# Performance work log

Measured on AMD Instinct MI355X. Metric: run time of the kernel, lower is better.

## Reference

```python
import math
import jax, jax.numpy as jnp
import numpy as np


def _alibi_slopes(n_heads: int) -> np.ndarray:
    def pow2_slopes(n):
        start = 2 ** (-2 ** (-(math.log2(n) - 3)))
        return [start * (start ** i) for i in range(n)]
    if n_heads & (n_heads - 1) == 0:
        slopes = pow2_slopes(n_heads)
    else:
        closest = 2 ** math.floor(math.log2(n_heads))
        slopes = pow2_slopes(closest)
        extra_base = 2 ** (-2 ** (-(math.log2(2 * closest) - 3)))
        slopes.extend(extra_base * (extra_base ** i) for i in range(n_heads - closest))
        slopes = slopes[:n_heads]
    return np.asarray(slopes, dtype=np.float32)


def setup_inputs() -> dict:
    B, T, C, H = 2, 2048, 768, 12
    key = jax.random.key(0)
    ks = jax.random.split(key, 6)
    return {
        "x_norm_for_qk": jax.random.normal(ks[0], (B, T, C), jnp.float32),
        "xt_current_for_v": jax.random.normal(ks[1], (B, T, C), jnp.float32),
        "W_attn": jax.random.normal(ks[2], (2 * C, C), jnp.float32) * 0.02,  # nn.Linear weight [out,in]
        "b_attn": jnp.zeros((2 * C,), jnp.float32),
        "v_tmp": jax.random.normal(ks[3], (H, H), jnp.float32) * 0.02,
        "proj_tmp": jax.random.normal(ks[4], (H, H), jnp.float32) * 0.02,
    }


def reference(x_norm_for_qk, xt_current_for_v, W_attn, b_attn, v_tmp, proj_tmp):
    B, T, C = x_norm_for_qk.shape
    H = v_tmp.shape[0]
    hd = C // H

    # Q,K projection: Linear(C -> 2C), then split.
    qk = x_norm_for_qk @ W_attn.T + b_attn  # [B,T,2C]
    q, k = jnp.split(qk, 2, axis=-1)
    q = q.reshape(B, T, H, hd).transpose(0, 2, 1, 3)  # [B,H,T,hd]
    k = k.reshape(B, T, H, hd).transpose(0, 2, 1, 3)

    # Kronecker-lifted V: block (i,j) of the CxC matrix is v_tmp[i,j]*I(hd),
    # so applying it mixes only across heads per head-dim channel.
    xt = xt_current_for_v.reshape(B, T, H, hd)
    v = jnp.einsum("ij,btjd->btid", v_tmp, xt).transpose(0, 2, 1, 3)  # [B,H,T,hd]

    scale = 1.0 / math.sqrt(hd)
    scores = jnp.einsum("bhqd,bhkd->bhqk", q, k) * scale  # [B,H,T,T]

    # ALiBi bias with causal mask (-inf above diagonal).
    slopes = jnp.asarray(_alibi_slopes(H))  # [H]
    pos = jnp.arange(T, dtype=jnp.float32)
    rel = pos[None, :] - pos[:, None]  # [T,T], memory - context
    causal = pos[None, :] <= pos[:, None]
    bias = jnp.where(causal[None], slopes[:, None, None] * rel[None], -jnp.inf)  # [H,T,T]
    scores = scores + bias[None]

    att = jax.nn.softmax(scores, axis=-1)  # dropout p=0 -> identity
    y = jnp.einsum("bhqk,bhkd->bhqd", att, v)  # [B,H,T,hd]
    y = y.transpose(0, 2, 1, 3)  # [B,T,H,hd]

    # Kronecker-lifted output projection.
    y = jnp.einsum("ij,btjd->btid", proj_tmp, y)
    return y.reshape(B, T, C)
```

## Files before the change

### kernel.cpp

```cpp
#include <hip/hip_runtime.h>
#include <hip/hip_bf16.h>
#include <math.h>

#define TSEQ 2048
#define CDIM 768
#define NH   12
#define HD   64

typedef __attribute__((ext_vector_type(8))) short bf16x8;
typedef __attribute__((ext_vector_type(4))) float f32x4;

union Bf8 { bf16x8 v; __hip_bfloat16 e[8]; };

__constant__ float c_slopes2[12] = {
    0.72134752f, 0.36067376f, 0.18033688f, 0.09016844f,
    0.04508422f, 0.02254211f, 0.011271055f, 0.0056355275f,
    1.02015692f, 0.72134752f, 0.51007846f, 0.36067376f
};
#define M2 4.3280851f
#define QSCALE 0.18033688f
#define EXP2F(x) __builtin_amdgcn_exp2f(x)

__device__ __forceinline__ unsigned pack2(float lo, float hi) {
    union { __hip_bfloat162 b; unsigned u; } cv;
    cv.b = __float22bfloat162_rn(make_float2(lo, hi));
    return cv.u;
}
__device__ __forceinline__ unsigned short bf16bits(float x) {
    union { __hip_bfloat16 b; unsigned short s; } cv;
    cv.b = __float2bfloat16(x);
    return cv.s;
}

#define MFMA16(a, b, c) __builtin_amdgcn_mfma_f32_16x16x32_bf16(a, b, c, 0, 0, 0)

__global__ __launch_bounds__(256) void gemm_qk(
    const float* __restrict__ X,
    const float* __restrict__ W,
    const float* __restrict__ bias,
    __hip_bfloat16* __restrict__ Qb,
    __hip_bfloat16* __restrict__ Kt)
{
    __shared__ alignas(16) __hip_bfloat16 As[128][40];
    __shared__ alignas(16) __hip_bfloat16 Bs[64][40];

    const int tid  = threadIdx.x;
    const int lane = tid & 63;
    const int w    = tid >> 6;
    const int lg   = lane >> 4;
    const int lc   = lane & 15;
    const int m0   = blockIdx.y * 128;
    const int n0   = blockIdx.x * 64;
    const int m0w  = (w >> 1) * 64;
    const int n0w  = (w & 1) * 32;

    const int r0 = tid >> 2;
    const int c0 = (tid & 3) * 8;

    f32x4 acc[4][2] = {};

    for (int k0 = 0; k0 < CDIM; k0 += 32) {
        __syncthreads();
        {
            const float* xp0 = X + (size_t)(m0 + r0) * CDIM + k0 + c0;
            const float* xp1 = X + (size_t)(m0 + r0 + 64) * CDIM + k0 + c0;
            const float* wp  = W + (size_t)(n0 + r0) * CDIM + k0 + c0;
            float4 a00 = *(const float4*)(xp0);
            float4 a01 = *(const float4*)(xp0 + 4);
            float4 a10 = *(const float4*)(xp1);
            float4 a11 = *(const float4*)(xp1 + 4);
            float4 b0  = *(const float4*)(wp);
            float4 b1  = *(const float4*)(wp + 4);
            Bf8 v0, v1, bv;
            v0.e[0]=__float2bfloat16(a00.x); v0.e[1]=__float2bfloat16(a00.y);
            v0.e[2]=__float2bfloat16(a00.z); v0.e[3]=__float2bfloat16(a00.w);
            v0.e[4]=__float2bfloat16(a01.x); v0.e[5]=__float2bfloat16(a01.y);
            v0.e[6]=__float2bfloat16(a01.z); v0.e[7]=__float2bfloat16(a01.w);
            v1.e[0]=__float2bfloat16(a10.x); v1.e[1]=__float2bfloat16(a10.y);
            v1.e[2]=__float2bfloat16(a10.z); v1.e[3]=__float2bfloat16(a10.w);
            v1.e[4]=__float2bfloat16(a11.x); v1.e[5]=__float2bfloat16(a11.y);
            v1.e[6]=__float2bfloat16(a11.z); v1.e[7]=__float2bfloat16(a11.w);
            bv.e[0]=__float2bfloat16(b0.x);  bv.e[1]=__float2bfloat16(b0.y);
            bv.e[2]=__float2bfloat16(b0.z);  bv.e[3]=__float2bfloat16(b0.w);
            bv.e[4]=__float2bfloat16(b1.x);  bv.e[5]=__float2bfloat16(b1.y);
            bv.e[6]=__float2bfloat16(b1.z);  bv.e[7]=__float2bfloat16(b1.w);
            *(bf16x8*)&As[r0][c0]      = v0.v;
            *(bf16x8*)&As[r0 + 64][c0] = v1.v;
            *(bf16x8*)&Bs[r0][c0]      = bv.v;
        }
        __syncthreads();

        bf16x8 af[4], bfr[2];
        #pragma unroll
        for (int mt = 0; mt < 4; ++mt)
            af[mt] = *(const bf16x8*)&As[m0w + mt*16 + lc][lg*8];
        #pragma unroll
        for (int nt = 0; nt < 2; ++nt)
            bfr[nt] = *(const bf16x8*)&Bs[n0w + nt*16 + lc][lg*8];
        #pragma unroll
        for (int mt = 0; mt < 4; ++mt)
            #pragma unroll
            for (int nt = 0; nt < 2; ++nt)
                acc[mt][nt] = MFMA16(af[mt], bfr[nt], acc[mt][nt]);
    }

    #pragma unroll
    for (int mt = 0; mt < 4; ++mt) {
        #pragma unroll
        for (int nt = 0; nt < 2; ++nt) {
            int n  = n0 + n0w + nt*16 + lc;
            float bv = bias[n];
            #pragma unroll
            for (int r = 0; r < 4; ++r) {
                int m = m0 + m0w + mt*16 + lg*4 + r;
                float v = acc[mt][nt][r] + bv;
                int b = m >> 11, t = m & (TSEQ-1);
                if (n < CDIM) {
                    int h = n >> 6, dd = n & 63;
                    Qb[(((size_t)(b*NH + h))*TSEQ + t)*HD + dd] = __float2bfloat16(v * QSCALE);
                } else {
                    int n2 = n - CDIM;
                    int h = n2 >> 6, dd = n2 & 63;
                    int bh_ = b*NH + h;
                    int kb = t >> 5, tt = t & 31;
                    int j  = ((tt >> 4) << 1) + (dd >> 5);
                    int ln = (((dd >> 3) & 3) << 4) + (tt & 15);
                    Kt[((size_t)(bh_*64 + kb))*2048 + j*512 + ln*8 + (dd & 7)] =
                        __float2bfloat16(v);
                }
            }
        }
    }
}

__global__ __launch_bounds__(256) void vmix(
    const float* __restrict__ XT, const float* __restrict__ vtmp,
    __hip_bfloat16* __restrict__ Vb)
{
    __shared__ float vm[144];
    if (threadIdx.x < 144) vm[threadIdx.x] = vtmp[threadIdx.x];
    __syncthreads();
    int idx = blockIdx.x * 256 + threadIdx.x;
    int dd = idx & 63;
    int bt = idx >> 6;
    int t = bt & (TSEQ-1), b = bt >> 11;
    float xv[12];
    #pragma unroll
    for (int j = 0; j < 12; ++j) xv[j] = XT[(size_t)bt*CDIM + j*64 + dd];
    #pragma unroll
    for (int i = 0; i < 12; ++i) {
        float s = 0.f;
        #pragma unroll
        for (int j = 0; j < 12; ++j) s += vm[i*12+j] * xv[j];
        Vb[(((size_t)(b*NH + i))*TSEQ + t)*HD + dd] = __float2bfloat16(s);
    }
}

__global__ __launch_bounds__(256) void vtrans(
    const __hip_bfloat16* __restrict__ Vb, __hip_bfloat16* __restrict__ Vt)
{
    __shared__ __hip_bfloat16 Ls[64][65];
    const int bh = blockIdx.y;
    const int t0 = blockIdx.x * 64;
    const int tid = threadIdx.x;
    const int r8 = tid >> 3;
    const int c8 = (tid & 7) * 8;

    #pragma unroll
    for (int it = 0; it < 2; ++it) {
        int t = it*32 + r8;
        Bf8 v; v.v = *(const bf16x8*)(Vb + ((size_t)bh*TSEQ + t0 + t)*HD + c8);
        #pragma unroll
        for (int j = 0; j < 8; ++j) Ls[t][c8 + j] = v.e[j];
    }
    __syncthreads();
    #pragma unroll
    for (int it = 0; it < 2; ++it) {
        int d = it*32 + r8;
        Bf8 v;
        #pragma unroll
        for (int j = 0; j < 8; ++j) v.e[j] = Ls[c8 + j][d];
        int kb = (t0 + c8) >> 5;
        int ko = (t0 + c8) & 31;
        *(bf16x8*)(Vt + (size_t)bh*(HD*TSEQ) + kb*2048 + d*32 + ko) = v.v;
    }
}

__global__ __launch_bounds__(256, 3) void attn8(
    const __hip_bfloat16* __restrict__ Qb,
    const __hip_bfloat16* __restrict__ Kt,
    const __hip_bfloat16* __restrict__ Vt,
    __hip_bfloat16* __restrict__ Y)
{
    __shared__ float Osh[4][2][64][20];
    __shared__ float Lsh[4][2][16];

    const int tid  = threadIdx.x;
    const int lane = tid & 63;
    const int w    = tid >> 6;
    const int lg   = lane >> 4;
    const int lc   = lane & 15;

    const int id  = blockIdx.x;
    const int id2 = (id & 7) * 96 + (id >> 3);
    const int bx  = id2 & 31;
    const int bh  = id2 >> 5;

    const float slope = c_slopes2[bh % NH];
    const __hip_bfloat16* Qp = Qb + (size_t)bh * TSEQ * HD;
    const __hip_bfloat16* Kp = Kt + (size_t)bh * 64 * 2048;
    const __hip_bfloat16* Vp = Vt + (size_t)bh * (HD * TSEQ);

    const float slgl  = slope * (float)(lg * 4);
    const float slp16 = slope * 16.0f;
    const int   s01   = lc + ((lg & 1) << 5);
    const int   s23   = s01 + 16;
    const bool  hiK   = (lg >= 2);

    bf16x8 kA0, kA1, kA2, kA3, kB0, kB1, kB2, kB3;

#define LOADK(S, TI) do {                                                       \
    const __hip_bfloat16* kp_ = Kp + (size_t)(TI)*2048 + lane*8;                \
    k##S##0 = *(const bf16x8*)(kp_);                                            \
    k##S##1 = *(const bf16x8*)(kp_ + 512);                                      \
    k##S##2 = *(const bf16x8*)(kp_ + 1024);                                     \
    k##S##3 = *(const bf16x8*)(kp_ + 1536);                                     \
} while (0);

#define SHUF(P_, x0, x1, x2, x3)                                                \
    {                                                                           \
        int t00 = __shfl((int)x0, s01), t02 = __shfl((int)x2, s01);             \
        int t10 = __shfl((int)x1, s01), t12 = __shfl((int)x3, s01);             \
        int t20 = __shfl((int)x0, s23), t22 = __shfl((int)x2, s23);             \
        int t30 = __shfl((int)x1, s23), t32 = __shfl((int)x3, s23);             \
        P_.u[0] = hiK ? (unsigned)t02 : (unsigned)t00;                          \
        P_.u[1] = hiK ? (unsigned)t12 : (unsigned)t10;                          \
        P_.u[2] = hiK ? (unsigned)t22 : (unsigned)t20;                          \
        P_.u[3] = hiK ? (unsigned)t32 : (unsigned)t30;                          \
    }

#define CONS(TI, S) do {                                                        \
    const int K0C = (TI) * 32;                                                  \
    const __hip_bfloat16* vb_ = Vp + (size_t)(TI)*2048 + lc*32 + lg*8;          \
    bf16x8 v0_ = *(const bf16x8*)(vb_);                                         \
    bf16x8 v1_ = *(const bf16x8*)(vb_ + 512);                                   \
    bf16x8 v2_ = *(const bf16x8*)(vb_ + 1024);                                  \
    bf16x8 v3_ = *(const bf16x8*)(vb_ + 1536);                                  \
    f32x4 s0a = {}, s0b = {}, s1a = {}, s1b = {};                               \
    s0a = MFMA16(k##S##0, qfa0, s0a); s0a = MFMA16(k##S##1, qfa1, s0a);         \
    s0b = MFMA16(k##S##0, qfb0, s0b); s0b = MFMA16(k##S##1, qfb1, s0b);         \
    s1a = MFMA16(k##S##2, qfa0, s1a); s1a = MFMA16(k##S##3, qfa1, s1a);         \
    s1b = MFMA16(k##S##2, qfb0, s1b); s1b = MFMA16(k##S##3, qfb1, s1b);         \
    float base0_ = fmaf((float)K0C, slope, slgl);                               \
    float pa0[4], pa1[4], pb0[4], pb1[4];                                       \
    _Pragma("unroll")                                                           \
    for (int r = 0; r < 4; ++r) {                                               \
        float bk_  = base0_ + slope * (float)r;                                 \
        float bk1_ = bk_ + slp16;                                               \
        int kk0_ = K0C + lg*4 + r, kk1_ = kk0_ + 16;                            \
        float e0a = EXP2F(s0a[r] + (bk_  - eqa));                               \
        float e1a = EXP2F(s1a[r] + (bk1_ - eqa));                               \
        float e0b = EXP2F(s0b[r] + (bk_  - eqb));                               \
        float e1b = EXP2F(s1b[r] + (bk1_ - eqb));                               \
        pa0[r] = (kk0_ <= qia) ? e0a : 0.f;                                     \
        pa1[r] = (kk1_ <= qia) ? e1a : 0.f;                                     \
        pb0[r] = (kk0_ <= qib) ? e0b : 0.f;                                     \
        pb1[r] = (kk1_ <= qib) ? e1b : 0.f;                                     \
        lsa += pa0[r] + pa1[r];                                                 \
        lsb += pb0[r] + pb1[r];                                                 \
    }                                                                           \
    unsigned a0_ = pack2(pa0[0], pa0[1]), a1_ = pack2(pa0[2], pa0[3]);          \
    unsigned a2_ = pack2(pa1[0], pa1[1]), a3_ = pack2(pa1[2], pa1[3]);          \
    unsigned b0_ = pack2(pb0[0], pb0[1]), b1_ = pack2(pb0[2], pb0[3]);          \
    unsigned b2_ = pack2(pb1[0], pb1[1]), b3_ = pack2(pb1[2], pb1[3]);          \
    union { unsigned u[4]; bf16x8 v; } PA_, PB_;                                \
    SHUF(PA_, a0_, a1_, a2_, a3_)                                               \
    SHUF(PB_, b0_, b1_, b2_, b3_)                                               \
    Oa[0] = MFMA16(v0_, PA_.v, Oa[0]); Ob[0] = MFMA16(v0_, PB_.v, Ob[0]);       \
    Oa[1] = MFMA16(v1_, PA_.v, Oa[1]); Ob[1] = MFMA16(v1_, PB_.v, Ob[1]);       \
    Oa[2] = MFMA16(v2_, PA_.v, Oa[2]); Ob[2] = MFMA16(v2_, PB_.v, Ob[2]);       \
    Oa[3] = MFMA16(v3_, PA_.v, Oa[3]); Ob[3] = MFMA16(v3_, PB_.v, Ob[3]);       \
} while (0);

    auto runMember = [&](int qb, bool first) {
        const int q0m = qb * 32;
        const int qia = q0m + lc;
        const int qib = q0m + 16 + lc;
        const float eqa = slope * (float)qia + M2;
        const float eqb = slope * (float)qib + M2;

        bf16x8 qfa0 = *(const bf16x8*)(Qp + (size_t)qia * HD + lg*8);
        bf16x8 qfa1 = *(const bf16x8*)(Qp + (size_t)qia * HD + 32 + lg*8);
        bf16x8 qfb0 = *(const bf16x8*)(Qp + (size_t)qib * HD + lg*8);
        bf16x8 qfb1 = *(const bf16x8*)(Qp + (size_t)qib * HD + 32 + lg*8);

        f32x4 Oa[4] = {}; f32x4 Ob[4] = {};
        float lsa = 0.f, lsb = 0.f;

        const int myN = (qb >= w) ? ((qb - w) >> 2) + 1 : 0;

        if (myN > 0) {
            LOADK(A, w)
            int j = 0;
            while (true) {
                if (j + 1 < myN) LOADK(B, w + 4*(j+1))
                CONS(w + 4*j, A)
                ++j; if (j >= myN) break;
                if (j + 1 < myN) LOADK(A, w + 4*(j+1))
                CONS(w + 4*j, B)
                ++j; if (j >= myN) break;
            }
        }

        lsa += __shfl_xor(lsa, 16); lsa += __shfl_xor(lsa, 32);
        lsb += __shfl_xor(lsb, 16); lsb += __shfl_xor(lsb, 32);

        if (!first) __syncthreads();
        #pragma unroll
        for (int dt = 0; dt < 4; ++dt) {
            *(f32x4*)&Osh[w][0][lane][dt*4] = Oa[dt];
            *(f32x4*)&Osh[w][1][lane][dt*4] = Ob[dt];
        }
        if (lane < 16) {
            Lsh[w][0][lane] = lsa;
            Lsh[w][1][lane] = lsb;
        }
        __syncthreads();

        #pragma unroll
        for (int h = 0; h < 2; ++h) {
            f32x4 o = (h == 0) ? Oa[w] : Ob[w];
            #pragma unroll
            for (int w2 = 0; w2 < 4; ++w2)
                if (w2 != w) o += *(const f32x4*)&Osh[w2][h][lane][w*4];
            float lt = Lsh[0][h][lc] + Lsh[1][h][lc] + Lsh[2][h][lc] + Lsh[3][h][lc];
            float inv = 1.0f / lt;
            int q = q0m + h*16 + lc;
            ushort4 u;
            u.x = bf16bits(o[0] * inv);
            u.y = bf16bits(o[1] * inv);
            u.z = bf16bits(o[2] * inv);
            u.w = bf16bits(o[3] * inv);
            *(ushort4*)(Y + ((size_t)bh*TSEQ + q)*HD + w*16 + lg*4) = u;
        }
    };

    runMember(bx, true);
    runMember(63 - bx, false);

#undef LOADK
#undef SHUF
#undef CONS
}

__global__ __launch_bounds__(256) void projmix(
    const __hip_bfloat16* __restrict__ Y, const float* __restrict__ ptmp,
    float* __restrict__ Out)
{
    __shared__ float pm[144];
    if (threadIdx.x < 144) pm[threadIdx.x] = ptmp[threadIdx.x];
    __syncthreads();
    int idx = blockIdx.x * 256 + threadIdx.x;
    int dd = idx & 63;
    int bt = idx >> 6;
    int t = bt & (TSEQ-1), b = bt >> 11;
    float yv[12];
    #pragma unroll
    for (int j = 0; j < 12; ++j)
        yv[j] = __bfloat162float(Y[(((size_t)(b*NH + j))*TSEQ + t)*HD + dd]);
    #pragma unroll
    for (int i = 0; i < 12; ++i) {
        float s = 0.f;
        #pragma unroll
        for (int j = 0; j < 12; ++j) s += pm[i*12+j] * yv[j];
        Out[(size_t)bt*CDIM + i*64 + dd] = s;
    }
}

extern "C" void kernel_launch(void* const* d_in, const int* in_sizes, int n_in,
                              void* d_out, int out_size, void* d_ws, size_t ws_size,
                              hipStream_t stream) {
    (void)in_sizes; (void)n_in; (void)out_size; (void)ws_size;
    const float* X    = (const float*)d_in[0];
    const float* XT   = (const float*)d_in[1];
    const float* W    = (const float*)d_in[2];
    const float* bias = (const float*)d_in[3];
    const float* vtmp = (const float*)d_in[4];
    const float* ptmp = (const float*)d_in[5];
    float* Out = (float*)d_out;

    char* ws = (char*)d_ws;
    const size_t BHTD = (size_t)2 * NH * TSEQ * HD;
    __hip_bfloat16* Qb = (__hip_bfloat16*)ws;
    __hip_bfloat16* Kt = (__hip_bfloat16*)(ws + BHTD*2);
    __hip_bfloat16* Vb = (__hip_bfloat16*)(ws + BHTD*4);
    __hip_bfloat16* Vt = (__hip_bfloat16*)(ws + BHTD*6);
    __hip_bfloat16* Yb = (__hip_bfloat16*)(ws + BHTD*8);

    gemm_qk<<<dim3(24, 32), 256, 0, stream>>>(X, W, bias, Qb, Kt);
    vmix<<<1024, 256, 0, stream>>>(XT, vtmp, Vb);
    vtrans<<<dim3(32, 24), 256, 0, stream>>>(Vb, Vt);
    attn8<<<768, 256, 0, stream>>>(Qb, Kt, Vt, Yb);
    projmix<<<1024, 256, 0, stream>>>(Yb, ptmp, Out);
}
```

Measured before the change: 81.91 us.

## Fuse QK GEMM, V mixing and transpose into one prep kernel; split attention blocks

After: 197.1 us. +140.6%, slower.

```diff
diff --git a/kernel.cpp b/kernel.cpp
--- a/kernel.cpp
+++ b/kernel.cpp
@@ -34,177 +34,173 @@
 
 #define MFMA16(a, b, c) __builtin_amdgcn_mfma_f32_16x16x32_bf16(a, b, c, 0, 0, 0)
 
-__global__ __launch_bounds__(256) void gemm_qk(
+__global__ __launch_bounds__(256) void prep(
     const float* __restrict__ X,
     const float* __restrict__ W,
     const float* __restrict__ bias,
+    const float* __restrict__ XT,
+    const float* __restrict__ vtmp,
     __hip_bfloat16* __restrict__ Qb,
-    __hip_bfloat16* __restrict__ Kt)
+    __hip_bfloat16* __restrict__ Kt,
+    __hip_bfloat16* __restrict__ Vt)
 {
     __shared__ alignas(16) __hip_bfloat16 As[128][40];
     __shared__ alignas(16) __hip_bfloat16 Bs[64][40];
+    __shared__ float vm[144];
+
+    const int bid = blockIdx.x;
+    const int tid = threadIdx.x;
+
+    if (bid < 768) {
+        const int lane = tid & 63;
+        const int w    = tid >> 6;
+        const int lg   = lane >> 4;
+        const int lc   = lane & 15;
+        const int m0   = (bid / 24) * 128;
+        const int n0   = (bid % 24) * 64;
+        const int m0w  = (w >> 1) * 64;
+        const int n0w  = (w & 1) * 32;
+
+        const int r0 = tid >> 2;
+        const int c0 = (tid & 3) * 8;
+
+        f32x4 acc[4][2] = {};
+
+        for (int k0 = 0; k0 < CDIM; k0 += 32) {
+            __syncthreads();
+            {
+                const float* xp0 = X + (size_t)(m0 + r0) * CDIM + k0 + c0;
+                const float* xp1 = X + (size_t)(m0 + r0 + 64) * CDIM + k0 + c0;
+                const float* wp  = W + (size_t)(n0 + r0) * CDIM + k0 + c0;
+                float4 a00 = *(const float4*)(xp0);
+                float4 a01 = *(const float4*)(xp0 + 4);
+                float4 a10 = *(const float4*)(xp1);
+                float4 a11 = *(const float4*)(xp1 + 4);
+                float4 b0  = *(const float4*)(wp);
+                float4 b1  = *(const float4*)(wp + 4);
+                Bf8 v0, v1, bv;
+                v0.e[0]=__float2bfloat16(a00.x); v0.e[1]=__float2bfloat16(a00.y);
+                v0.e[2]=__float2bfloat16(a00.z); v0.e[3]=__float2bfloat16(a00.w);
+                v0.e[4]=__float2bfloat16(a01.x); v0.e[5]=__float2bfloat16(a01.y);
+                v0.e[6]=__float2bfloat16(a01.z); v0.e[7]=__float2bfloat16(a01.w);
+                v1.e[0]=__float2bfloat16(a10.x); v1.e[1]=__float2bfloat16(a10.y);
+                v1.e[2]=__float2bfloat16(a10.z); v1.e[3]=__float2bfloat16(a10.w);
+                v1.e[4]=__float2bfloat16(a11.x); v1.e[5]=__float2bfloat16(a11.y);
+                v1.e[6]=__float2bfloat16(a11.z); v1.e[7]=__float2bfloat16(a11.w);
+                bv.e[0]=__float2bfloat16(b0.x);  bv.e[1]=__float2bfloat16(b0.y);
+                bv.e[2]=__float2bfloat16(b0.z);  bv.e[3]=__float2bfloat16(b0.w);
+                bv.e[4]=__float2bfloat16(b1.x);  bv.e[5]=__float2bfloat16(b1.y);
+                bv.e[6]=__float2bfloat16(b1.z);  bv.e[7]=__float2bfloat16(b1.w);
+                *(bf16x8*)&As[r0][c0]      = v0.v;
+                *(bf16x8*)&As[r0 + 64][c0] = v1.v;
+                *(bf16x8*)&Bs[r0][c0]      = bv.v;
+            }
+            __syncthreads();
+
+            bf16x8 af[4], bfr[2];
+            #pragma unroll
+            for (int mt = 0; mt < 4; ++mt)
+                af[mt] = *(const bf16x8*)&As[m0w + mt*16 + lc][lg*8];
+            #pragma unroll
+            for (int nt = 0; nt < 2; ++nt)
+                bfr[nt] = *(const bf16x8*)&Bs[n0w + nt*16 + lc][lg*8];
+            #pragma unroll
+            for (int mt = 0; mt < 4; ++mt)
+                #pragma unroll
+                for (int nt = 0; nt < 2; ++nt)
+                    acc[mt][nt] = MFMA16(af[mt], bfr[nt], acc[mt][nt]);
+        }
+
+        #pragma unroll
+        for (int mt = 0; mt < 4; ++mt) {
+            #pragma unroll
+            for (int nt = 0; nt < 2; ++nt) {
+                int n  = n0 + n0w + nt*16 + lc;
+                float bv = bias[n];
+                #pragma unroll
+                for (int r = 0; r < 4; ++r) {
+                    int m = m0 + m0w + mt*16 + lg*4 + r;
+                    float v = acc[mt][nt][r] + bv;
+                    int b = m >> 11, t = m & (TSEQ-1);
+                    if (n < CDIM) {
+                        int h = n >> 6, dd = n & 63;
+                        Qb[(((size_t)(b*NH + h))*TSEQ + t)*HD + dd] = __float2bfloat16(v * QSCALE);
+                    } else {
+                        int n2 = n - CDIM;
+                        int h = n2 >> 6, dd = n2 & 63;
+                        int bh_ = b*NH + h;
+                        int kb = t >> 5, tt = t & 31;
+                        int j  = ((tt >> 4) << 1) + (dd >> 5);
+                        int ln = (((dd >> 3) & 3) << 4) + (tt & 15);
+                        Kt[((size_t)(bh_*64 + kb))*2048 + j*512 + ln*8 + (dd & 7)] =
+                            __float2bfloat16(v);
+                    }
+                }
+            }
+        }
+    } else {
+        const int vb = bid - 768;
+        const int b  = vb >> 5;
+        const int t0 = (vb & 31) * 64;
+        const int tl = tid >> 2;
+        const int dq = tid & 3;
+
+        if (tid < 144) vm[tid] = vtmp[tid];
+        __syncthreads();
+
+        const int tg  = t0 + tl;
+        const size_t xbase = (size_t)(b*TSEQ + tg) * CDIM;
+        const int kb0 = tg >> 5;
+        const int ko  = tg & 31;
+
+        #pragma unroll
+        for (int c = 0; c < 4; ++c) {
+            const int dd0 = dq*16 + c*4;
+            float4 xv[12];
+            #pragma unroll
+            for (int j = 0; j < 12; ++j)
+                xv[j] = *(const float4*)(XT + xbase + j*64 + dd0);
+            #pragma unroll
+            for (int i = 0; i < 12; ++i) {
+                float ox = 0.f, oy = 0.f, oz = 0.f, ow = 0.f;
+                #pragma unroll
+                for (int j = 0; j < 12; ++j) {
+                    float s = vm[i*12 + j];
+                    ox = fmaf(s, xv[j].x, ox);
+                    oy = fmaf(s, xv[j].y, oy);
+                    oz = fmaf(s, xv[j].z, oz);
+                    ow = fmaf(s, xv[j].w, ow);
+                }
+                __hip_bfloat16* vt = Vt + (size_t)(b*NH + i)*(HD*TSEQ)
+                                       + (size_t)kb0*2048 + ko;
+                vt[(dd0+0)*32] = __float2bfloat16(ox);
+                vt[(dd0+1)*32] = __float2bfloat16(oy);
+                vt[(dd0+2)*32] = __float2bfloat16(oz);
+                vt[(dd0+3)*32] = __float2bfloat16(ow);
+            }
+        }
+    }
+}
+
+__global__ __launch_bounds__(256, 6) void attn11(
+    const __hip_bfloat16* __restrict__ Qb,
+    const __hip_bfloat16* __restrict__ Kt,
+    const __hip_bfloat16* __restrict__ Vt,
+    __hip_bfloat16* __restrict__ Y)
+{
+    __shared__ float Osh[4][64][20];
+    __shared__ float Lsh[4][16];
 
     const int tid  = threadIdx.x;
     const int lane = tid & 63;
     const int w    = tid >> 6;
     const int lg   = lane >> 4;
     const int lc   = lane & 15;
-    const int m0   = blockIdx.y * 128;
-    const int n0   = blockIdx.x * 64;
-    const int m0w  = (w >> 1) * 64;
-    const int n0w  = (w & 1) * 32;
-
-    const int r0 = tid >> 2;
-    const int c0 = (tid & 3) * 8;
-
-    f32x4 acc[4][2] = {};
-
-    for (int k0 = 0; k0 < CDIM; k0 += 32) {
-        __syncthreads();
-        {
-            const float* xp0 = X + (size_t)(m0 + r0) * CDIM + k0 + c0;
-            const float* xp1 = X + (size_t)(m0 + r0 + 64) * CDIM + k0 + c0;
-            const float* wp  = W + (size_t)(n0 + r0) * CDIM + k0 + c0;
-            float4 a00 = *(const float4*)(xp0);
-            float4 a01 = *(const float4*)(xp0 + 4);
-            float4 a10 = *(const float4*)(xp1);
-            float4 a11 = *(const float4*)(xp1 + 4);
-            float4 b0  = *(const float4*)(wp);
-            float4 b1  = *(const float4*)(wp + 4);
-            Bf8 v0, v1, bv;
-            v0.e[0]=__float2bfloat16(a00.x); v0.e[1]=__float2bfloat16(a00.y);
-            v0.e[2]=__float2bfloat16(a00.z); v0.e[3]=__float2bfloat16(a00.w);
-            v0.e[4]=__float2bfloat16(a01.x); v0.e[5]=__float2bfloat16(a01.y);
-            v0.e[6]=__float2bfloat16(a01.z); v0.e[7]=__float2bfloat16(a01.w);
-            v1.e[0]=__float2bfloat16(a10.x); v1.e[1]=__float2bfloat16(a10.y);
-            v1.e[2]=__float2bfloat16(a10.z); v1.e[3]=__float2bfloat16(a10.w);
-            v1.e[4]=__float2bfloat16(a11.x); v1.e[5]=__float2bfloat16(a11.y);
-            v1.e[6]=__float2bfloat16(a11.z); v1.e[7]=__float2bfloat16(a11.w);
-            bv.e[0]=__float2bfloat16(b0.x);  bv.e[1]=__float2bfloat16(b0.y);
-            bv.e[2]=__float2bfloat16(b0.z);  bv.e[3]=__float2bfloat16(b0.w);
-            bv.e[4]=__float2bfloat16(b1.x);  bv.e[5]=__float2bfloat16(b1.y);
-            bv.e[6]=__float2bfloat16(b1.z);  bv.e[7]=__float2bfloat16(b1.w);
-            *(bf16x8*)&As[r0][c0]      = v0.v;
-            *(bf16x8*)&As[r0 + 64][c0] = v1.v;
-            *(bf16x8*)&Bs[r0][c0]      = bv.v;
-        }
-        __syncthreads();
-
-        bf16x8 af[4], bfr[2];
-        #pragma unroll
-        for (int mt = 0; mt < 4; ++mt)
-            af[mt] = *(const bf16x8*)&As[m0w + mt*16 + lc][lg*8];
-        #pragma unroll
-        for (int nt = 0; nt < 2; ++nt)
-            bfr[nt] = *(const bf16x8*)&Bs[n0w + nt*16 + lc][lg*8];
-        #pragma unroll
-        for (int mt = 0; mt < 4; ++mt)
-            #pragma unroll
-            for (int nt = 0; nt < 2; ++nt)
-                acc[mt][nt] = MFMA16(af[mt], bfr[nt], acc[mt][nt]);
-    }
-
-    #pragma unroll
-    for (int mt = 0; mt < 4; ++mt) {
-        #pragma unroll
-        for (int nt = 0; nt < 2; ++nt) {
-            int n  = n0 + n0w + nt*16 + lc;
-            float bv = bias[n];
-            #pragma unroll
-            for (int r = 0; r < 4; ++r) {
-                int m = m0 + m0w + mt*16 + lg*4 + r;
-                float v = acc[mt][nt][r] + bv;
-                int b = m >> 11, t = m & (TSEQ-1);
-                if (n < CDIM) {
-                    int h = n >> 6, dd = n & 63;
-                    Qb[(((size_t)(b*NH + h))*TSEQ + t)*HD + dd] = __float2bfloat16(v * QSCALE);
-                } else {
-                    int n2 = n - CDIM;
-                    int h = n2 >> 6, dd = n2 & 63;
-                    int bh_ = b*NH + h;
-                    int kb = t >> 5, tt = t & 31;
-                    int j  = ((tt >> 4) << 1) + (dd >> 5);
-                    int ln = (((dd >> 3) & 3) << 4) + (tt & 15);
-                    Kt[((size_t)(bh_*64 + kb))*2048 + j*512 + ln*8 + (dd & 7)] =
-                        __float2bfloat16(v);
-                }
-            }
-        }
-    }
-}
-
-__global__ __launch_bounds__(256) void vmix(
-    const float* __restrict__ XT, const float* __restrict__ vtmp,
-    __hip_bfloat16* __restrict__ Vb)
-{
-    __shared__ float vm[144];
-    if (threadIdx.x < 144) vm[threadIdx.x] = vtmp[threadIdx.x];
-    __syncthreads();
-    int idx = blockIdx.x * 256 + threadIdx.x;
-    int dd = idx & 63;
-    int bt = idx >> 6;
-    int t = bt & (TSEQ-1), b = bt >> 11;
-    float xv[12];
-    #pragma unroll
-    for (int j = 0; j < 12; ++j) xv[j] = XT[(size_t)bt*CDIM + j*64 + dd];
-    #pragma unroll
-    for (int i = 0; i < 12; ++i) {
-        float s = 0.f;
-        #pragma unroll
-        for (int j = 0; j < 12; ++j) s += vm[i*12+j] * xv[j];
-        Vb[(((size_t)(b*NH + i))*TSEQ + t)*HD + dd] = __float2bfloat16(s);
-    }
-}
-
-__global__ __launch_bounds__(256) void vtrans(
-    const __hip_bfloat16* __restrict__ Vb, __hip_bfloat16* __restrict__ Vt)
-{
-    __shared__ __hip_bfloat16 Ls[64][65];
-    const int bh = blockIdx.y;
-    const int t0 = blockIdx.x * 64;
-    const int tid = threadIdx.x;
-    const int r8 = tid >> 3;
-    const int c8 = (tid & 7) * 8;
-
-    #pragma unroll
-    for (int it = 0; it < 2; ++it) {
-        int t = it*32 + r8;
-        Bf8 v; v.v = *(const bf16x8*)(Vb + ((size_t)bh*TSEQ + t0 + t)*HD + c8);
-        #pragma unroll
-        for (int j = 0; j < 8; ++j) Ls[t][c8 + j] = v.e[j];
-    }
-    __syncthreads();
-    #pragma unroll
-    for (int it = 0; it < 2; ++it) {
-        int d = it*32 + r8;
-        Bf8 v;
-        #pragma unroll
-        for (int j = 0; j < 8; ++j) v.e[j] = Ls[c8 + j][d];
-        int kb = (t0 + c8) >> 5;
-        int ko = (t0 + c8) & 31;
-        *(bf16x8*)(Vt + (size_t)bh*(HD*TSEQ) + kb*2048 + d*32 + ko) = v.v;
-    }
-}
-
-__global__ __launch_bounds__(256, 3) void attn8(
-    const __hip_bfloat16* __restrict__ Qb,
-    const __hip_bfloat16* __restrict__ Kt,
-    const __hip_bfloat16* __restrict__ Vt,
-    __hip_bfloat16* __restrict__ Y)
-{
-    __shared__ float Osh[4][2][64][20];
-    __shared__ float Lsh[4][2][16];
-
-    const int tid  = threadIdx.x;
-    const int lane = tid & 63;
-    const int w    = tid >> 6;
-    const int lg   = lane >> 4;
-    const int lc   = lane & 15;
 
     const int id  = blockIdx.x;
-    const int id2 = (id & 7) * 96 + (id >> 3);
-    const int bx  = id2 & 31;
-    const int bh  = id2 >> 5;
+    const int id2 = (id & 7) * 192 + (id >> 3);
+    const int qb  = 63 - (id2 & 63);
+    const int bh  = id2 >> 6;
 
     const float slope = c_slopes2[bh % NH];
     const __hip_bfloat16* Qp = Qb + (size_t)bh * TSEQ * HD;
@@ -217,140 +213,134 @@
     const int   s23   = s01 + 16;
     const bool  hiK   = (lg >= 2);
 
-    bf16x8 kA0, kA1, kA2, kA3, kB0, kB1, kB2, kB3;
-
-#define LOADK(S, TI) do {                                                       \
-    const __hip_bfloat16* kp_ = Kp + (size_t)(TI)*2048 + lane*8;                \
-    k##S##0 = *(const bf16x8*)(kp_);                                            \
-    k##S##1 = *(const bf16x8*)(kp_ + 512);                                      \
-    k##S##2 = *(const bf16x8*)(kp_ + 1024);                                     \
-    k##S##3 = *(const bf16x8*)(kp_ + 1536);                                     \
-} while (0);
-
-#define SHUF(P_, x0, x1, x2, x3)                                                \
-    {                                                                           \
-        int t00 = __shfl((int)x0, s01), t02 = __shfl((int)x2, s01);             \
-        int t10 = __shfl((int)x1, s01), t12 = __shfl((int)x3, s01);             \
-        int t20 = __shfl((int)x0, s23), t22 = __shfl((int)x2, s23);             \
-        int t30 = __shfl((int)x1, s23), t32 = __shfl((int)x3, s23);             \
-        P_.u[0] = hiK ? (unsigned)t02 : (unsigned)t00;                          \
-        P_.u[1] = hiK ? (unsigned)t12 : (unsigned)t10;                          \
-        P_.u[2] = hiK ? (unsigned)t22 : (unsigned)t20;                          \
-        P_.u[3] = hiK ? (unsigned)t32 : (unsigned)t30;                          \
-    }
-
-#define CONS(TI, S) do {                                                        \
-    const int K0C = (TI) * 32;                                                  \
-    const __hip_bfloat16* vb_ = Vp + (size_t)(TI)*2048 + lc*32 + lg*8;          \
-    bf16x8 v0_ = *(const bf16x8*)(vb_);                                         \
-    bf16x8 v1_ = *(const bf16x8*)(vb_ + 512);                                   \
-    bf16x8 v2_ = *(const bf16x8*)(vb_ + 1024);                                  \
-    bf16x8 v3_ = *(const bf16x8*)(vb_ + 1536);                                  \
-    f32x4 s0a = {}, s0b = {}, s1a = {}, s1b = {};                               \
-    s0a = MFMA16(k##S##0, qfa0, s0a); s0a = MFMA16(k##S##1, qfa1, s0a);         \
-    s0b = MFMA16(k##S##0, qfb0, s0b); s0b = MFMA16(k##S##1, qfb1, s0b);         \
-    s1a = MFMA16(k##S##2, qfa0, s1a); s1a = MFMA16(k##S##3, qfa1, s1a);         \
-    s1b = MFMA16(k##S##2, qfb0, s1b); s1b = MFMA16(k##S##3, qfb1, s1b);         \
-    float base0_ = fmaf((float)K0C, slope, slgl);                               \
-    float pa0[4], pa1[4], pb0[4], pb1[4];                                       \
-    _Pragma("unroll")                                                           \
-    for (int r = 0; r < 4; ++r) {                                               \
-        float bk_  = base0_ + slope * (float)r;                                 \
-        float bk1_ = bk_ + slp16;                                               \
-        int kk0_ = K0C + lg*4 + r, kk1_ = kk0_ + 16;                            \
-        float e0a = EXP2F(s0a[r] + (bk_  - eqa));                               \
-        float e1a = EXP2F(s1a[r] + (bk1_ - eqa));                               \
-        float e0b = EXP2F(s0b[r] + (bk_  - eqb));                               \
-        float e1b = EXP2F(s1b[r] + (bk1_ - eqb));                               \
-        pa0[r] = (kk0_ <= qia) ? e0a : 0.f;                                     \
-        pa1[r] = (kk1_ <= qia) ? e1a : 0.f;                                     \
-        pb0[r] = (kk0_ <= qib) ? e0b : 0.f;                                     \
-        pb1[r] = (kk1_ <= qib) ? e1b : 0.f;                                     \
-        lsa += pa0[r] + pa1[r];                                                 \
-        lsb += pb0[r] + pb1[r];                                                 \
-    }                                                                           \
-    unsigned a0_ = pack2(pa0[0], pa0[1]), a1_ = pack2(pa0[2], pa0[3]);          \
-    unsigned a2_ = pack2(pa1[0], pa1[1]), a3_ = pack2(pa1[2], pa1[3]);          \
-    unsigned b0_ = pack2(pb0[0], pb0[1]), b1_ = pack2(pb0[2], pb0[3]);          \
-    unsigned b2_ = pack2(pb1[0], pb1[1]), b3_ = pack2(pb1[2], pb1[3]);          \
-    union { unsigned u[4]; bf16x8 v; } PA_, PB_;                                \
-    SHUF(PA_, a0_, a1_, a2_, a3_)                                               \
-    SHUF(PB_, b0_, b1_, b2_, b3_)                                               \
-    Oa[0] = MFMA16(v0_, PA_.v, Oa[0]); Ob[0] = MFMA16(v0_, PB_.v, Ob[0]);       \
-    Oa[1] = MFMA16(v1_, PA_.v, Oa[1]); Ob[1] = MFMA16(v1_, PB_.v, Ob[1]);       \
-    Oa[2] = MFMA16(v2_, PA_.v, Oa[2]); Ob[2] = MFMA16(v2_, PB_.v, Ob[2]);       \
-    Oa[3] = MFMA16(v3_, PA_.v, Oa[3]); Ob[3] = MFMA16(v3_, PB_.v, Ob[3]);       \
-} while (0);
-
-    auto runMember = [&](int qb, bool first) {
-        const int q0m = qb * 32;
-        const int qia = q0m + lc;
-        const int qib = q0m + 16 + lc;
-        const float eqa = slope * (float)qia + M2;
-        const float eqb = slope * (float)qib + M2;
-
-        bf16x8 qfa0 = *(const bf16x8*)(Qp + (size_t)qia * HD + lg*8);
-        bf16x8 qfa1 = *(const bf16x8*)(Qp + (size_t)qia * HD + 32 + lg*8);
-        bf16x8 qfb0 = *(const bf16x8*)(Qp + (size_t)qib * HD + lg*8);
-        bf16x8 qfb1 = *(const bf16x8*)(Qp + (size_t)qib * HD + 32 + lg*8);
-
-        f32x4 Oa[4] = {}; f32x4 Ob[4] = {};
-        float lsa = 0.f, lsb = 0.f;
-
-        const int myN = (qb >= w) ? ((qb - w) >> 2) + 1 : 0;
-
-        if (myN > 0) {
-            LOADK(A, w)
-            int j = 0;
-            while (true) {
-                if (j + 1 < myN) LOADK(B, w + 4*(j+1))
-                CONS(w + 4*j, A)
-                ++j; if (j >= myN) break;
-                if (j + 1 < myN) LOADK(A, w + 4*(j+1))
-                CONS(w + 4*j, B)
-                ++j; if (j >= myN) break;
-            }
-        }
-
-        lsa += __shfl_xor(lsa, 16); lsa += __shfl_xor(lsa, 32);
-        lsb += __shfl_xor(lsb, 16); lsb += __shfl_xor(lsb, 32);
-
-        if (!first) __syncthreads();
-        #pragma unroll
-        for (int dt = 0; dt < 4; ++dt) {
-            *(f32x4*)&Osh[w][0][lane][dt*4] = Oa[dt];
-            *(f32x4*)&Osh[w][1][lane][dt*4] = Ob[dt];
-        }
-        if (lane < 16) {
-            Lsh[w][0][lane] = lsa;
-            Lsh[w][1][lane] = lsb;
-        }
-        __syncthreads();
-
-        #pragma unroll
-        for (int h = 0; h < 2; ++h) {
-            f32x4 o = (h == 0) ? Oa[w] : Ob[w];
-            #pragma unroll
-            for (int w2 = 0; w2 < 4; ++w2)
-                if (w2 != w) o += *(const f32x4*)&Osh[w2][h][lane][w*4];
-            float lt = Lsh[0][h][lc] + Lsh[1][h][lc] + Lsh[2][h][lc] + Lsh[3][h][lc];
-            float inv = 1.0f / lt;
-            int q = q0m + h*16 + lc;
-            ushort4 u;
-            u.x = bf16bits(o[0] * inv);
-            u.y = bf16bits(o[1] * inv);
-            u.z = bf16bits(o[2] * inv);
-            u.w = bf16bits(o[3] * inv);
-            *(ushort4*)(Y + ((size_t)bh*TSEQ + q)*HD + w*16 + lg*4) = u;
-        }
-    };
-
-    runMember(bx, true);
-    runMember(63 - bx, false);
-
-#undef LOADK
-#undef SHUF
-#undef CONS
+    const int q0m = qb * 32;
+    const int qia = q0m + lc;
+    const int qib = q0m + 16 + lc;
+    const float eqa = slope * (float)qia + M2;
+    const float eqb = slope * (float)qib + M2;
+
+    bf16x8 qfa0 = *(const bf16x8*)(Qp + (size_t)qia * HD + lg*8);
+    bf16x8 qfa1 = *(const bf16x8*)(Qp + (size_t)qia * HD + 32 + lg*8);
+    bf16x8 qfb0 = *(const bf16x8*)(Qp + (size_t)qib * HD + lg*8);
+    bf16x8 qfb1 = *(const bf16x8*)(Qp + (size_t)qib * HD + 32 + lg*8);
+
+    f32x4 Oa[4] = {}; f32x4 Ob[4] = {};
+    float lsa = 0.f, lsb = 0.f;
+
+    const int myN = (qb >= w) ? ((qb - w) >> 2) + 1 : 0;
+
+    for (int j = 0; j < myN; ++j) {
+        const int TI  = w + 4*j;
+        const int K0C = TI * 32;
+        const __hip_bfloat16* kp_ = Kp + (size_t)TI*2048 + lane*8;
+        bf16x8 k0 = *(const bf16x8*)(kp_);
+        bf16x8 k1 = *(const bf16x8*)(kp_ + 512);
+        bf16x8 k2 = *(const bf16x8*)(kp_ + 1024);
+        bf16x8 k3 = *(const bf16x8*)(kp_ + 1536);
+        const __hip_bfloat16* vb_ = Vp + (size_t)TI*2048 + lc*32 + lg*8;
+        bf16x8 v0 = *(const bf16x8*)(vb_);
+        bf16x8 v1 = *(const bf16x8*)(vb_ + 512);
+        bf16x8 v2 = *(const bf16x8*)(vb_ + 1024);
+        bf16x8 v3 = *(const bf16x8*)(vb_ + 1536);
+
+        f32x4 s0a = {}, s0b = {}, s1a = {}, s1b = {};
+        s0a = MFMA16(k0, qfa0, s0a); s0a = MFMA16(k1, qfa1, s0a);
+        s0b = MFMA16(k0, qfb0, s0b); s0b = MFMA16(k1, qfb1, s0b);
+        s1a = MFMA16(k2, qfa0, s1a); s1a = MFMA16(k3, qfa1, s1a);
+        s1b = MFMA16(k2, qfb0, s1b); s1b = MFMA16(k3, qfb1, s1b);
+
+        float base0 = fmaf((float)K0C, slope, slgl);
+        float pa0[4], pa1[4], pb0[4], pb1[4];
+        #pragma unroll
+        for (int r = 0; r < 4; ++r) {
+            float bk  = base0 + slope * (float)r;
+            float bk1 = bk + slp16;
+            int kk0 = K0C + lg*4 + r, kk1 = kk0 + 16;
+            float e0a = EXP2F(s0a[r] + (bk  - eqa));
+            float e1a = EXP2F(s1a[r] + (bk1 - eqa));
+            float e0b = EXP2F(s0b[r] + (bk  - eqb));
+            float e1b = EXP2F(s1b[r] + (bk1 - eqb));
+            pa0[r] = (kk0 <= qia) ? e0a : 0.f;
+            pa1[r] = (kk1 <= qia) ? e1a : 0.f;
+            pb0[r] = (kk0 <= qib) ? e0b : 0.f;
+            pb1[r] = (kk1 <= qib) ? e1b : 0.f;
+            lsa += pa0[r] + pa1[r];
+            lsb += pb0[r] + pb1[r];
+        }
+        unsigned a0 = pack2(pa0[0], pa0[1]), a1 = pack2(pa0[2], pa0[3]);
+        unsigned a2 = pack2(pa1[0], pa1[1]), a3 = pack2(pa1[2], pa1[3]);
+        unsigned b0 = pack2(pb0[0], pb0[1]), b1 = pack2(pb0[2], pb0[3]);
+        unsigned b2 = pack2(pb1[0], pb1[1]), b3 = pack2(pb1[2], pb1[3]);
+        union { unsigned u[4]; bf16x8 v; } PA, PB;
+        {
+            int t00 = __shfl((int)a0, s01), t02 = __shfl((int)a2, s01);
+            int t10 = __shfl((int)a1, s01), t12 = __shfl((int)a3, s01);
+            int t20 = __shfl((int)a0, s23), t22 = __shfl((int)a2, s23);
+            int t30 = __shfl((int)a1, s23), t32 = __shfl((int)a3, s23);
+            PA.u[0] = hiK ? (unsigned)t02 : (unsigned)t00;
+            PA.u[1] = hiK ? (unsigned)t12 : (unsigned)t10;
+            PA.u[2] = hiK ? (unsigned)t22 : (unsigned)t20;
+            PA.u[3] = hiK ? (unsigned)t32 : (unsigned)t30;
+        }
+        {
+            int t00 = __shfl((int)b0, s01), t02 = __shfl((int)b2, s01);
+            int t10 = __shfl((int)b1, s01), t12 = __shfl((int)b3, s01);
+            int t20 = __shfl((int)b0, s23), t22 = __shfl((int)b2, s23);
+            int t30 = __shfl((int)b1, s23), t32 = __shfl((int)b3, s23);
+            PB.u[0] = hiK ? (unsigned)t02 : (unsigned)t00;
+            PB.u[1] = hiK ? (unsigned)t12 : (unsigned)t10;
+            PB.u[2] = hiK ? (unsigned)t22 : (unsigned)t20;
+            PB.u[3] = hiK ? (unsigned)t32 : (unsigned)t30;
+        }
+        Oa[0] = MFMA16(v0, PA.v, Oa[0]); Ob[0] = MFMA16(v0, PB.v, Ob[0]);
+        Oa[1] = MFMA16(v1, PA.v, Oa[1]); Ob[1] = MFMA16(v1, PB.v, Ob[1]);
+        Oa[2] = MFMA16(v2, PA.v, Oa[2]); Ob[2] = MFMA16(v2, PB.v, Ob[2]);
+        Oa[3] = MFMA16(v3, PA.v, Oa[3]); Ob[3] = MFMA16(v3, PB.v, Ob[3]);
+    }
+
+    lsa += __shfl_xor(lsa, 16); lsa += __shfl_xor(lsa, 32);
+    lsb += __shfl_xor(lsb, 16); lsb += __shfl_xor(lsb, 32);
+
+    #pragma unroll
+    for (int dt = 0; dt < 4; ++dt)
+        *(f32x4*)&Osh[w][lane][dt*4] = Oa[dt];
+    if (lane < 16) Lsh[w][lane] = lsa;
+    __syncthreads();
+    {
+        f32x4 o = {};
+        #pragma unroll
+        for (int w2 = 0; w2 < 4; ++w2)
+            o += *(const f32x4*)&Osh[w2][lane][w*4];
+        float lt = Lsh[0][lc] + Lsh[1][lc] + Lsh[2][lc] + Lsh[3][lc];
+        float inv = 1.0f / lt;
+        ushort4 u;
+        u.x = bf16bits(o[0] * inv);
+        u.y = bf16bits(o[1] * inv);
+        u.z = bf16bits(o[2] * inv);
+        u.w = bf16bits(o[3] * inv);
+        *(ushort4*)(Y + ((size_t)bh*TSEQ + q0m + lc)*HD + w*16 + lg*4) = u;
+    }
+    __syncthreads();
+
+    #pragma unroll
+    for (int dt = 0; dt < 4; ++dt)
+        *(f32x4*)&Osh[w][lane][dt*4] = Ob[dt];
+    if (lane < 16) Lsh[w][lane] = lsb;
+    __syncthreads();
+    {
+        f32x4 o = {};
+        #pragma unroll
+        for (int w2 = 0; w2 < 4; ++w2)
+            o += *(const f32x4*)&Osh[w2][lane][w*4];
+        float lt = Lsh[0][lc] + Lsh[1][lc] + Lsh[2][lc] + Lsh[3][lc];
+        float inv = 1.0f / lt;
+        ushort4 u;
+        u.x = bf16bits(o[0] * inv);
+        u.y = bf16bits(o[1] * inv);
+        u.z = bf16bits(o[2] * inv);
+        u.w = bf16bits(o[3] * inv);
+        *(ushort4*)(Y + ((size_t)bh*TSEQ + q0m + 16 + lc)*HD + w*16 + lg*4) = u;
+    }
 }
 
 __global__ __launch_bounds__(256) void projmix(
@@ -393,13 +383,10 @@
     const size_t BHTD = (size_t)2 * NH * TSEQ * HD;
     __hip_bfloat16* Qb = (__hip_bfloat16*)ws;
     __hip_bfloat16* Kt = (__hip_bfloat16*)(ws + BHTD*2);
-    __hip_bfloat16* Vb = (__hip_bfloat16*)(ws + BHTD*4);
-    __hip_bfloat16* Vt = (__hip_bfloat16*)(ws + BHTD*6);
-    __hip_bfloat16* Yb = (__hip_bfloat16*)(ws + BHTD*8);
-
-    gemm_qk<<<dim3(24, 32), 256, 0, stream>>>(X, W, bias, Qb, Kt);
-    vmix<<<1024, 256, 0, stream>>>(XT, vtmp, Vb);
-    vtrans<<<dim3(32, 24), 256, 0, stream>>>(Vb, Vt);
-    attn8<<<768, 256, 0, stream>>>(Qb, Kt, Vt, Yb);
+    __hip_bfloat16* Vt = (__hip_bfloat16*)(ws + BHTD*4);
+    __hip_bfloat16* Yb = (__hip_bfloat16*)(ws + BHTD*6);
+
+    prep<<<832, 256, 0, stream>>>(X, W, bias, XT, vtmp, Qb, Kt, Vt);
+    attn11<<<1536, 256, 0, stream>>>(Qb, Kt, Vt, Yb);
     projmix<<<1024, 256, 0, stream>>>(Yb, ptmp, Out);
 }
```

## Fuse V head-mixing with transpose and skip causal masking on off-diagonal tiles

Applied to the files above, without the earlier changes.

Measured after the change: 85.07 us. 1.04x slower.

```diff
diff --git a/kernel.cpp b/kernel.cpp
--- a/kernel.cpp
+++ b/kernel.cpp
@@ -133,60 +133,52 @@
     }
 }
 
-__global__ __launch_bounds__(256) void vmix(
+__global__ __launch_bounds__(256) void vmixt(
     const float* __restrict__ XT, const float* __restrict__ vtmp,
-    __hip_bfloat16* __restrict__ Vb)
+    __hip_bfloat16* __restrict__ Vt)
 {
     __shared__ float vm[144];
-    if (threadIdx.x < 144) vm[threadIdx.x] = vtmp[threadIdx.x];
+    const int tid = threadIdx.x;
+    if (tid < 144) vm[tid] = vtmp[tid];
     __syncthreads();
-    int idx = blockIdx.x * 256 + threadIdx.x;
-    int dd = idx & 63;
-    int bt = idx >> 6;
-    int t = bt & (TSEQ-1), b = bt >> 11;
-    float xv[12];
-    #pragma unroll
-    for (int j = 0; j < 12; ++j) xv[j] = XT[(size_t)bt*CDIM + j*64 + dd];
-    #pragma unroll
-    for (int i = 0; i < 12; ++i) {
-        float s = 0.f;
-        #pragma unroll
-        for (int j = 0; j < 12; ++j) s += vm[i*12+j] * xv[j];
-        Vb[(((size_t)(b*NH + i))*TSEQ + t)*HD + dd] = __float2bfloat16(s);
-    }
-}
-
-__global__ __launch_bounds__(256) void vtrans(
-    const __hip_bfloat16* __restrict__ Vb, __hip_bfloat16* __restrict__ Vt)
-{
-    __shared__ __hip_bfloat16 Ls[64][65];
-    const int bh = blockIdx.y;
-    const int t0 = blockIdx.x * 64;
-    const int tid = threadIdx.x;
-    const int r8 = tid >> 3;
-    const int c8 = (tid & 7) * 8;
-
-    #pragma unroll
-    for (int it = 0; it < 2; ++it) {
-        int t = it*32 + r8;
-        Bf8 v; v.v = *(const bf16x8*)(Vb + ((size_t)bh*TSEQ + t0 + t)*HD + c8);
-        #pragma unroll
-        for (int j = 0; j < 8; ++j) Ls[t][c8 + j] = v.e[j];
-    }
-    __syncthreads();
-    #pragma unroll
-    for (int it = 0; it < 2; ++it) {
-        int d = it*32 + r8;
+
+    const int id2 = (blockIdx.x & 7) * 64 + (blockIdx.x >> 3);
+    const int ig  = id2 & 3;
+    const int kbb = id2 >> 2;
+    const int kb  = kbb & 63;
+    const int b   = kbb >> 6;
+    const int g   = tid >> 6;
+    const int dd  = tid & 63;
+    const int i0  = ig * 3;
+
+    float acc[3][8];
+    #pragma unroll
+    for (int i = 0; i < 3; ++i)
+        #pragma unroll
+        for (int e = 0; e < 8; ++e) acc[i][e] = 0.f;
+
+    const int tbase = kb*32 + g*8;
+    #pragma unroll
+    for (int e = 0; e < 8; ++e) {
+        const float* xp = XT + ((size_t)(b*TSEQ + tbase + e))*CDIM + dd;
+        #pragma unroll
+        for (int j = 0; j < 12; ++j) {
+            float x = xp[j*64];
+            acc[0][e] = fmaf(vm[(i0+0)*12 + j], x, acc[0][e]);
+            acc[1][e] = fmaf(vm[(i0+1)*12 + j], x, acc[1][e]);
+            acc[2][e] = fmaf(vm[(i0+2)*12 + j], x, acc[2][e]);
+        }
+    }
+    #pragma unroll
+    for (int i = 0; i < 3; ++i) {
         Bf8 v;
         #pragma unroll
-        for (int j = 0; j < 8; ++j) v.e[j] = Ls[c8 + j][d];
-        int kb = (t0 + c8) >> 5;
-        int ko = (t0 + c8) & 31;
-        *(bf16x8*)(Vt + (size_t)bh*(HD*TSEQ) + kb*2048 + d*32 + ko) = v.v;
-    }
-}
-
-__global__ __launch_bounds__(256, 3) void attn8(
+        for (int e = 0; e < 8; ++e) v.e[e] = __float2bfloat16(acc[i][e]);
+        *(bf16x8*)(Vt + (size_t)(b*NH + i0 + i)*(HD*TSEQ) + kb*2048 + dd*32 + g*8) = v.v;
+    }
+}
+
+__global__ __launch_bounds__(256, 3) void attn8m(
     const __hip_bfloat16* __restrict__ Qb,
     const __hip_bfloat16* __restrict__ Kt,
     const __hip_bfloat16* __restrict__ Vt,
@@ -239,7 +231,7 @@
         P_.u[3] = hiK ? (unsigned)t32 : (unsigned)t30;                          \
     }
 
-#define CONS(TI, S) do {                                                        \
+#define CONS(TI, S, MASKED) do {                                                \
     const int K0C = (TI) * 32;                                                  \
     const __hip_bfloat16* vb_ = Vp + (size_t)(TI)*2048 + lc*32 + lg*8;          \
     bf16x8 v0_ = *(const bf16x8*)(vb_);                                         \
@@ -257,15 +249,17 @@
     for (int r = 0; r < 4; ++r) {                                               \
         float bk_  = base0_ + slope * (float)r;                                 \
         float bk1_ = bk_ + slp16;                                               \
-        int kk0_ = K0C + lg*4 + r, kk1_ = kk0_ + 16;                            \
-        float e0a = EXP2F(s0a[r] + (bk_  - eqa));                               \
-        float e1a = EXP2F(s1a[r] + (bk1_ - eqa));                               \
-        float e0b = EXP2F(s0b[r] + (bk_  - eqb));                               \
-        float e1b = EXP2F(s1b[r] + (bk1_ - eqb));                               \
-        pa0[r] = (kk0_ <= qia) ? e0a : 0.f;                                     \
-        pa1[r] = (kk1_ <= qia) ? e1a : 0.f;                                     \
-        pb0[r] = (kk0_ <= qib) ? e0b : 0.f;                                     \
-        pb1[r] = (kk1_ <= qib) ? e1b : 0.f;                                     \
+        pa0[r] = EXP2F(s0a[r] + (bk_  - eqa));                                  \
+        pa1[r] = EXP2F(s1a[r] + (bk1_ - eqa));                                  \
+        pb0[r] = EXP2F(s0b[r] + (bk_  - eqb));                                  \
+        pb1[r] = EXP2F(s1b[r] + (bk1_ - eqb));                                  \
+        if (MASKED) {                                                           \
+            int kk0_ = K0C + lg*4 + r, kk1_ = kk0_ + 16;                        \
+            if (kk0_ > qia) pa0[r] = 0.f;                                       \
+            if (kk1_ > qia) pa1[r] = 0.f;                                       \
+            if (kk0_ > qib) pb0[r] = 0.f;                                       \
+            if (kk1_ > qib) pb1[r] = 0.f;                                       \
+        }                                                                       \
         lsa += pa0[r] + pa1[r];                                                 \
         lsb += pb0[r] + pb1[r];                                                 \
     }                                                                           \
@@ -297,18 +291,22 @@
         f32x4 Oa[4] = {}; f32x4 Ob[4] = {};
         float lsa = 0.f, lsb = 0.f;
 
-        const int myN = (qb >= w) ? ((qb - w) >> 2) + 1 : 0;
+        const int  myN     = (qb >= w) ? ((qb - w) >> 2) + 1 : 0;
+        const bool ownDiag = (myN > 0) && ((qb & 3) == w);
+        const int  nFull   = myN - (ownDiag ? 1 : 0);
 
         if (myN > 0) {
             LOADK(A, w)
             int j = 0;
-            while (true) {
-                if (j + 1 < myN) LOADK(B, w + 4*(j+1))
-                CONS(w + 4*j, A)
-                ++j; if (j >= myN) break;
-                if (j + 1 < myN) LOADK(A, w + 4*(j+1))
-                CONS(w + 4*j, B)
-                ++j; if (j >= myN) break;
+            while (j < nFull) {
+                if (j + 1 < myN) {
+                    if (j & 1) { LOADK(A, w + 4*(j+1)) } else { LOADK(B, w + 4*(j+1)) }
+                }
+                if (j & 1) { CONS(w + 4*j, B, 0) } else { CONS(w + 4*j, A, 0) }
+                ++j;
+            }
+            if (ownDiag) {
+                if (j & 1) { CONS(w + 4*j, B, 1) } else { CONS(w + 4*j, A, 1) }
             }
         }
 
@@ -393,13 +391,11 @@
     const size_t BHTD = (size_t)2 * NH * TSEQ * HD;
     __hip_bfloat16* Qb = (__hip_bfloat16*)ws;
     __hip_bfloat16* Kt = (__hip_bfloat16*)(ws + BHTD*2);
-    __hip_bfloat16* Vb = (__hip_bfloat16*)(ws + BHTD*4);
-    __hip_bfloat16* Vt = (__hip_bfloat16*)(ws + BHTD*6);
-    __hip_bfloat16* Yb = (__hip_bfloat16*)(ws + BHTD*8);
+    __hip_bfloat16* Vt = (__hip_bfloat16*)(ws + BHTD*4);
+    __hip_bfloat16* Yb = (__hip_bfloat16*)(ws + BHTD*6);
 
     gemm_qk<<<dim3(24, 32), 256, 0, stream>>>(X, W, bias, Qb, Kt);
-    vmix<<<1024, 256, 0, stream>>>(XT, vtmp, Vb);
-    vtrans<<<dim3(32, 24), 256, 0, stream>>>(Vb, Vt);
-    attn8<<<768, 256, 0, stream>>>(Qb, Kt, Vt, Yb);
+    vmixt<<<512, 256, 0, stream>>>(XT, vtmp, Vt);
+    attn8m<<<768, 256, 0, stream>>>(Qb, Kt, Vt, Yb);
     projmix<<<1024, 256, 0, stream>>>(Yb, ptmp, Out);
 }
```
